# Performance work log

Hardware: AMD Instinct MI355X
Metric: run time of the kernel (lower is better)

Reference implementation:

```python
import jax, jax.numpy as jnp
import numpy as np

INPUT_DIM = 1024
HIDDEN_DIM = 512
SEQ_LEN = 512


def setup_inputs() -> dict:
    key = jax.random.key(0)
    ks = jax.random.split(key, 7)
    s = 1.0 / np.sqrt(INPUT_DIM)
    s2 = 1.0 / np.sqrt(HIDDEN_DIM)
    return {
        "vectors": jax.random.normal(ks[0], (1, SEQ_LEN, INPUT_DIM), dtype=jnp.float32),
        "W_h": jax.random.uniform(ks[1], (HIDDEN_DIM, INPUT_DIM), jnp.float32, -s, s),
        "b_h": jax.random.uniform(ks[2], (HIDDEN_DIM,), jnp.float32, -s, s),
        "W_m": jax.random.uniform(ks[3], (HIDDEN_DIM, INPUT_DIM), jnp.float32, -s, s),
        "b_m": jax.random.uniform(ks[4], (HIDDEN_DIM,), jnp.float32, -s, s),
        "w2": jax.random.uniform(ks[5], (HIDDEN_DIM,), jnp.float32, -s2, s2),
        "b2": jax.random.uniform(ks[6], (), jnp.float32, -s2, s2),
    }


def reference(vectors, W_h, b_h, W_m, b_m, w2, b2):
    # vectors: [1, S, D] -> squeeze leading batch dim (matches torch .squeeze(0))
    x = vectors[0]  # [S, D]
    # Two batched GEMMs replacing the per-token Python loop
    H = x @ W_h.T + b_h  # [S, Hd] head representations
    M = x @ W_m.T + b_m  # [S, Hd] modifier representations
    # Pairwise broadcast add + tanh + dot with layer_2 weights -> [S, S] scores
    pair = jnp.tanh(H[:, None, :] + M[None, :, :])  # [S, S, Hd]
    scores = jnp.einsum('hmd,d->hm', pair, w2) + b2
    return scores
```

## Files before the change

### kernel.cpp

```cpp
#include <hip/hip_runtime.h>

#define C2 2.8853900817779268f
#define DIN 1024
#define HD 512

typedef short short8 __attribute__((ext_vector_type(8)));
typedef float floatx4 __attribute__((ext_vector_type(4)));

__device__ __forceinline__ float rcp_fast(float x){ return __builtin_amdgcn_rcpf(x); }
__device__ __forceinline__ float exp2_fast(float x){ return __builtin_amdgcn_exp2f(x); }
__device__ __forceinline__ float comp4(const float4& v, int i){
    return i==0 ? v.x : i==1 ? v.y : i==2 ? v.z : v.w;
}
__device__ __forceinline__ unsigned short f2bf(float f){
    union{float f; unsigned int u;} v; v.f = f;
    unsigned int u = v.u;
    return (unsigned short)((u + 0x7FFFu + ((u >> 16) & 1u)) >> 16);
}

__global__ __launch_bounds__(256) void convert_kernel(
    const float* __restrict__ x, const float* __restrict__ Wh,
    const float* __restrict__ Wm, unsigned short* __restrict__ xb,
    unsigned short* __restrict__ whb, unsigned short* __restrict__ wmb)
{
    int r = blockIdx.z;
    const float* s = r == 0 ? x : r == 1 ? Wh : Wm;
    unsigned short* d = r == 0 ? xb : r == 1 ? whb : wmb;
    int i = (blockIdx.x * 256 + threadIdx.x) * 4;
    float4 v = *(const float4*)(s + i);
    ushort4 o = { f2bf(v.x), f2bf(v.y), f2bf(v.z), f2bf(v.w) };
    *(ushort4*)(d + i) = o;
}

__global__ __launch_bounds__(256) void mfma_gemm_kernel(
    const unsigned short* __restrict__ xb, const unsigned short* __restrict__ whb,
    const unsigned short* __restrict__ wmb, const float* __restrict__ bh,
    const float* __restrict__ bm, float* __restrict__ EH, float* __restrict__ EM)
{
    int mat = blockIdx.z;
    const unsigned short* B = mat ? wmb : whb;
    const float* bias = mat ? bm : bh;
    float* O = mat ? EM : EH;
    int j0 = blockIdx.x * 32, s0 = blockIdx.y * 32;
    int wave = threadIdx.x >> 6, lane = threadIdx.x & 63;
    int sw = (wave & 1) * 16, jw = (wave >> 1) * 16;
    int m = lane & 15, quad = lane >> 4;

    const unsigned short* ap = xb + (size_t)(s0 + sw + m) * DIN + quad * 8;
    const unsigned short* bp = B  + (size_t)(j0 + jw + m) * DIN + quad * 8;

    floatx4 acc = {0.f, 0.f, 0.f, 0.f};
    #pragma unroll 8
    for (int k = 0; k < DIN; k += 32){
        short8 af = *(const short8*)(ap + k);
        short8 bf = *(const short8*)(bp + k);
        acc = __builtin_amdgcn_mfma_f32_16x16x32_bf16(af, bf, acc, 0, 0, 0);
    }
    int col = j0 + jw + m;
    float bv = bias[col];
    #pragma unroll
    for (int i = 0; i < 4; i++){
        int row = s0 + sw + quad * 4 + i;
        O[(size_t)row * HD + col] = exp2_fast(C2 * (acc[i] + bv));
    }
}

__global__ __launch_bounds__(256, 4) void scores_kernel(
    const float* __restrict__ EH, const float* __restrict__ EM,
    const float* __restrict__ w2, float* __restrict__ Q)
{
    int m0 = blockIdx.x * 64, h0 = blockIdx.y * 32, d0 = blockIdx.z * 64;
    __shared__ float Hs[32 * 68];
    __shared__ float Ms[64 * 68];
    __shared__ float wsS[64];
    int tid = threadIdx.x;
    int tx = tid & 15, ty = tid >> 4;
    #pragma unroll
    for (int l = 0; l < 2; l++){
        int slot = tid + 256 * l;
        int row = slot >> 4, q = slot & 15;
        float4 h = *(const float4*)(EH + (size_t)(h0 + row) * HD + d0 + q * 4);
        *(float4*)&Hs[row * 68 + q * 4] = h;
    }
    #pragma unroll
    for (int l = 0; l < 4; l++){
        int slot = tid + 256 * l;
        int mm = slot >> 4, q = slot & 15;
        float4 v = *(const float4*)(EM + (size_t)(m0 + mm) * HD + d0 + q * 4);
        Ms[(q*4 + 0) * 68 + mm] = v.x;
        Ms[(q*4 + 1) * 68 + mm] = v.y;
        Ms[(q*4 + 2) * 68 + mm] = v.z;
        Ms[(q*4 + 3) * 68 + mm] = v.w;
    }
    if (tid < 16){
        float4 w = *(const float4*)(w2 + d0 + tid * 4);
        float4 ws = {-2.f * w.x, -2.f * w.y, -2.f * w.z, -2.f * w.w};
        *(float4*)&wsS[tid * 4] = ws;
    }
    __syncthreads();

    float acc[2][4] = {};
    #pragma unroll 2
    for (int it = 0; it < 16; it++){
        int dk = it * 4;
        float4 w4 = *(const float4*)&wsS[dk];
        float4 hA = *(const float4*)&Hs[(ty*2 + 0) * 68 + dk];
        float4 hB = *(const float4*)&Hs[(ty*2 + 1) * 68 + dk];
        #pragma unroll
        for (int dd = 0; dd < 4; dd++){
            float4 mv = *(const float4*)&Ms[(dk + dd) * 68 + tx * 4];
            float w = comp4(w4, dd);
            float e0 = comp4(hA, dd), e1 = comp4(hB, dd);
            acc[0][0] = fmaf(w, rcp_fast(fmaf(e0, mv.x, 1.f)), acc[0][0]);
            acc[0][1] = fmaf(w, rcp_fast(fmaf(e0, mv.y, 1.f)), acc[0][1]);
            acc[0][2] = fmaf(w, rcp_fast(fmaf(e0, mv.z, 1.f)), acc[0][2]);
            acc[0][3] = fmaf(w, rcp_fast(fmaf(e0, mv.w, 1.f)), acc[0][3]);
            acc[1][0] = fmaf(w, rcp_fast(fmaf(e1, mv.x, 1.f)), acc[1][0]);
            acc[1][1] = fmaf(w, rcp_fast(fmaf(e1, mv.y, 1.f)), acc[1][1]);
            acc[1][2] = fmaf(w, rcp_fast(fmaf(e1, mv.z, 1.f)), acc[1][2]);
            acc[1][3] = fmaf(w, rcp_fast(fmaf(e1, mv.w, 1.f)), acc[1][3]);
        }
    }
    float* Qp = Q + (size_t)blockIdx.z * 262144;
    #pragma unroll
    for (int i = 0; i < 2; i++){
        float4 v = {acc[i][0], acc[i][1], acc[i][2], acc[i][3]};
        *(float4*)&Qp[(h0 + ty*2 + i) * 512 + m0 + tx * 4] = v;
    }
}

__global__ __launch_bounds__(256) void combine_kernel(
    const float* __restrict__ Q, const float* __restrict__ w2,
    const float* __restrict__ b2, float* __restrict__ out)
{
    int tid = threadIdx.x;
    __shared__ float red[4];
    __shared__ float c0s;
    float s = 0.f;
    if (tid < 128){ float4 v = ((const float4*)w2)[tid]; s = v.x + v.y + v.z + v.w; }
    #pragma unroll
    for (int off = 32; off; off >>= 1) s += __shfl_down(s, off, 64);
    if (tid < 128 && (tid & 63) == 0) red[tid >> 6] = s;
    __syncthreads();
    if (tid == 0) c0s = red[0] + red[1] + b2[0];
    __syncthreads();
    float c0 = c0s;
    int g = blockIdx.x * 256 + tid;
    const float4* Q4 = (const float4*)Q;
    float4 a = Q4[g];
    #pragma unroll
    for (int sl = 1; sl < 8; sl++){
        float4 b = Q4[sl * 65536 + g];
        a.x += b.x; a.y += b.y; a.z += b.z; a.w += b.w;
    }
    float4 o = {a.x + c0, a.y + c0, a.z + c0, a.w + c0};
    ((float4*)out)[g] = o;
}

extern "C" void kernel_launch(void* const* d_in, const int* in_sizes, int n_in,
                              void* d_out, int out_size, void* d_ws, size_t ws_size,
                              hipStream_t stream) {
    const float* x   = (const float*)d_in[0];
    const float* Wh  = (const float*)d_in[1];
    const float* bh  = (const float*)d_in[2];
    const float* Wm  = (const float*)d_in[3];
    const float* bm  = (const float*)d_in[4];
    const float* w2  = (const float*)d_in[5];
    const float* b2  = (const float*)d_in[6];
    float* out = (float*)d_out;
    (void)in_sizes; (void)n_in; (void)out_size; (void)ws_size;

    float* w = (float*)d_ws;
    unsigned short* xb  = (unsigned short*)(w);
    unsigned short* whb = (unsigned short*)(w + 262144);
    unsigned short* wmb = (unsigned short*)(w + 524288);
    float* EH = w + 786432;
    float* EM = w + 1048576;
    float* Q  = w + 1310720;

    convert_kernel<<<dim3(512, 1, 3), 256, 0, stream>>>(x, Wh, Wm, xb, whb, wmb);
    mfma_gemm_kernel<<<dim3(16, 16, 2), 256, 0, stream>>>(xb, whb, wmb, bh, bm, EH, EM);
    scores_kernel<<<dim3(8, 16, 8), 256, 0, stream>>>(EH, EM, w2, Q);
    combine_kernel<<<256, 256, 0, stream>>>(Q, w2, b2, out);
}
```

Measured before the change: 109.2 us.

## Fuse split-K score partials and combine into single full-reduction scores kernel

The scores kernel now loops over the full hidden dimension in 64-wide chunks inside each block, accumulating directly instead of writing eight partial slices. The separate combine kernel and its partial-sum buffer are removed, with the w2-sum bias constant computed in-kernel. This removes the round trip of partials through memory and one launch. In exchange, blocks grow to 512 threads with 2 outputs per thread, so the grid shrinks and each thread does less work per shared-memory load, with two barriers per chunk.

```diff
diff --git a/kernel.cpp b/kernel.cpp
--- a/kernel.cpp
+++ b/kernel.cpp
@@ -65,96 +65,67 @@
     }
 }
 
-__global__ __launch_bounds__(256, 4) void scores_kernel(
+__global__ __launch_bounds__(512) void scores_kernel(
     const float* __restrict__ EH, const float* __restrict__ EM,
-    const float* __restrict__ w2, float* __restrict__ Q)
+    const float* __restrict__ w2, const float* __restrict__ b2,
+    float* __restrict__ out)
 {
-    int m0 = blockIdx.x * 64, h0 = blockIdx.y * 32, d0 = blockIdx.z * 64;
+    int m0 = blockIdx.x * 32, h0 = blockIdx.y * 32;
     __shared__ float Hs[32 * 68];
-    __shared__ float Ms[64 * 68];
+    __shared__ float Ms[64 * 34];
     __shared__ float wsS[64];
+    __shared__ float red[8];
+    __shared__ float c0s;
     int tid = threadIdx.x;
     int tx = tid & 15, ty = tid >> 4;
-    #pragma unroll
-    for (int l = 0; l < 2; l++){
-        int slot = tid + 256 * l;
-        int row = slot >> 4, q = slot & 15;
-        float4 h = *(const float4*)(EH + (size_t)(h0 + row) * HD + d0 + q * 4);
-        *(float4*)&Hs[row * 68 + q * 4] = h;
+
+    {
+        float s = 0.f;
+        if (tid < 128){ float4 v = ((const float4*)w2)[tid]; s = v.x + v.y + v.z + v.w; }
+        #pragma unroll
+        for (int off = 32; off; off >>= 1) s += __shfl_down(s, off, 64);
+        if ((tid & 63) == 0) red[tid >> 6] = s;
+        __syncthreads();
+        if (tid == 0) c0s = red[0] + red[1] + b2[0];
     }
-    #pragma unroll
-    for (int l = 0; l < 4; l++){
-        int slot = tid + 256 * l;
-        int mm = slot >> 4, q = slot & 15;
-        float4 v = *(const float4*)(EM + (size_t)(m0 + mm) * HD + d0 + q * 4);
-        Ms[(q*4 + 0) * 68 + mm] = v.x;
-        Ms[(q*4 + 1) * 68 + mm] = v.y;
-        Ms[(q*4 + 2) * 68 + mm] = v.z;
-        Ms[(q*4 + 3) * 68 + mm] = v.w;
-    }
-    if (tid < 16){
-        float4 w = *(const float4*)(w2 + d0 + tid * 4);
-        float4 ws = {-2.f * w.x, -2.f * w.y, -2.f * w.z, -2.f * w.w};
-        *(float4*)&wsS[tid * 4] = ws;
-    }
-    __syncthreads();
 
-    float acc[2][4] = {};
-    #pragma unroll 2
-    for (int it = 0; it < 16; it++){
-        int dk = it * 4;
-        float4 w4 = *(const float4*)&wsS[dk];
-        float4 hA = *(const float4*)&Hs[(ty*2 + 0) * 68 + dk];
-        float4 hB = *(const float4*)&Hs[(ty*2 + 1) * 68 + dk];
-        #pragma unroll
-        for (int dd = 0; dd < 4; dd++){
-            float4 mv = *(const float4*)&Ms[(dk + dd) * 68 + tx * 4];
-            float w = comp4(w4, dd);
-            float e0 = comp4(hA, dd), e1 = comp4(hB, dd);
-            acc[0][0] = fmaf(w, rcp_fast(fmaf(e0, mv.x, 1.f)), acc[0][0]);
-            acc[0][1] = fmaf(w, rcp_fast(fmaf(e0, mv.y, 1.f)), acc[0][1]);
-            acc[0][2] = fmaf(w, rcp_fast(fmaf(e0, mv.z, 1.f)), acc[0][2]);
-            acc[0][3] = fmaf(w, rcp_fast(fmaf(e0, mv.w, 1.f)), acc[0][3]);
-            acc[1][0] = fmaf(w, rcp_fast(fmaf(e1, mv.x, 1.f)), acc[1][0]);
-            acc[1][1] = fmaf(w, rcp_fast(fmaf(e1, mv.y, 1.f)), acc[1][1]);
-            acc[1][2] = fmaf(w, rcp_fast(fmaf(e1, mv.z, 1.f)), acc[1][2]);
-            acc[1][3] = fmaf(w, rcp_fast(fmaf(e1, mv.w, 1.f)), acc[1][3]);
+    float acc0 = 0.f, acc1 = 0.f;
+    for (int d0 = 0; d0 < 512; d0 += 64){
+        __syncthreads();
+        {
+            int row = tid >> 4, q = tid & 15;
+            float4 h = *(const float4*)(EH + (size_t)(h0 + row) * HD + d0 + q * 4);
+            *(float4*)&Hs[row * 68 + q * 4] = h;
+            int q2 = tid >> 5, mm = tid & 31;
+            float4 v = *(const float4*)(EM + (size_t)(m0 + mm) * HD + d0 + q2 * 4);
+            Ms[(q2*4 + 0) * 34 + mm] = v.x;
+            Ms[(q2*4 + 1) * 34 + mm] = v.y;
+            Ms[(q2*4 + 2) * 34 + mm] = v.z;
+            Ms[(q2*4 + 3) * 34 + mm] = v.w;
+            if (tid < 16){
+                float4 w = *(const float4*)(w2 + d0 + tid * 4);
+                float4 ws = {-2.f * w.x, -2.f * w.y, -2.f * w.z, -2.f * w.w};
+                *(float4*)&wsS[tid * 4] = ws;
+            }
+        }
+        __syncthreads();
+        #pragma unroll 4
+        for (int it = 0; it < 16; it++){
+            int dk = it * 4;
+            float4 w4 = *(const float4*)&wsS[dk];
+            float4 hA = *(const float4*)&Hs[ty * 68 + dk];
+            #pragma unroll
+            for (int dd = 0; dd < 4; dd++){
+                float2 mv = *(const float2*)&Ms[(dk + dd) * 34 + tx * 2];
+                float w = comp4(w4, dd), e = comp4(hA, dd);
+                acc0 = fmaf(w, rcp_fast(fmaf(e, mv.x, 1.f)), acc0);
+                acc1 = fmaf(w, rcp_fast(fmaf(e, mv.y, 1.f)), acc1);
+            }
         }
     }
-    float* Qp = Q + (size_t)blockIdx.z * 262144;
-    #pragma unroll
-    for (int i = 0; i < 2; i++){
-        float4 v = {acc[i][0], acc[i][1], acc[i][2], acc[i][3]};
-        *(float4*)&Qp[(h0 + ty*2 + i) * 512 + m0 + tx * 4] = v;
-    }
-}
-
-__global__ __launch_bounds__(256) void combine_kernel(
-    const float* __restrict__ Q, const float* __restrict__ w2,
-    const float* __restrict__ b2, float* __restrict__ out)
-{
-    int tid = threadIdx.x;
-    __shared__ float red[4];
-    __shared__ float c0s;
-    float s = 0.f;
-    if (tid < 128){ float4 v = ((const float4*)w2)[tid]; s = v.x + v.y + v.z + v.w; }
-    #pragma unroll
-    for (int off = 32; off; off >>= 1) s += __shfl_down(s, off, 64);
-    if (tid < 128 && (tid & 63) == 0) red[tid >> 6] = s;
-    __syncthreads();
-    if (tid == 0) c0s = red[0] + red[1] + b2[0];
-    __syncthreads();
-    float c0 = c0s;
-    int g = blockIdx.x * 256 + tid;
-    const float4* Q4 = (const float4*)Q;
-    float4 a = Q4[g];
-    #pragma unroll
-    for (int sl = 1; sl < 8; sl++){
-        float4 b = Q4[sl * 65536 + g];
-        a.x += b.x; a.y += b.y; a.z += b.z; a.w += b.w;
-    }
-    float4 o = {a.x + c0, a.y + c0, a.z + c0, a.w + c0};
-    ((float4*)out)[g] = o;
+    float c0v = c0s;
+    float2 o = {acc0 + c0v, acc1 + c0v};
+    *(float2*)&out[(size_t)(h0 + ty) * 512 + m0 + tx * 2] = o;
 }
 
 extern "C" void kernel_launch(void* const* d_in, const int* in_sizes, int n_in,
@@ -176,10 +147,8 @@
     unsigned short* wmb = (unsigned short*)(w + 524288);
     float* EH = w + 786432;
     float* EM = w + 1048576;
-    float* Q  = w + 1310720;
 
     convert_kernel<<<dim3(512, 1, 3), 256, 0, stream>>>(x, Wh, Wm, xb, whb, wmb);
     mfma_gemm_kernel<<<dim3(16, 16, 2), 256, 0, stream>>>(xb, whb, wmb, bh, bm, EH, EM);
-    scores_kernel<<<dim3(8, 16, 8), 256, 0, stream>>>(EH, EM, w2, Q);
-    combine_kernel<<<256, 256, 0, stream>>>(Q, w2, b2, out);
+    scores_kernel<<<dim3(16, 16), 512, 0, stream>>>(EH, EM, w2, b2, out);
 }
```

Result: slower. 113.9 us (+4.4%).
